# Optimization experiments

Measured on AMD Instinct MI355X. Metric: run time of the kernel, lower is better.

Reference implementation:

```python
import jax, jax.numpy as jnp
import numpy as np

K = 512
H = 8

def setup_inputs() -> dict:
    key = jax.random.key(0)
    k1, k2, k3, k4, k5 = jax.random.split(key, 5)
    b, s = 2, 2048
    x = jax.random.normal(k1, (b, s, K), dtype=jnp.float32)
    # torch Linear weights: shape [out_features, in_features]
    scale = 0.02
    Wq = jax.random.normal(k2, (H * K, K), dtype=jnp.float32) * scale
    Wk = jax.random.normal(k3, (H * K, K), dtype=jnp.float32) * scale
    Wv = jax.random.normal(k4, (H * K, K), dtype=jnp.float32) * scale
    Wu = jax.random.normal(k5, (K, H * K), dtype=jnp.float32) * scale
    return {"x": x, "Wq": Wq, "Wk": Wk, "Wv": Wv, "Wu": Wu}

def reference(x, Wq, Wk, Wv, Wu):
    b, s, _ = x.shape
    # project and split heads: [b, h, s, k]
    q = jnp.einsum('bsd,hed->bhse', x, Wq.reshape(H, K, K))
    kk = jnp.einsum('bsd,hed->bhse', x, Wk.reshape(H, K, K))
    v = jnp.einsum('bsd,hed->bhse', x, Wv.reshape(H, K, K))
    scale = K ** (-0.25)
    dot = jnp.einsum('bhse,bhte->bhst', q * scale, kk * scale)  # [b,h,s,s]
    causal = jnp.tril(jnp.ones((s, s), dtype=bool))
    dot = jnp.where(causal[None, None], dot, -jnp.inf)
    weights = jax.nn.softmax(dot, axis=-1)
    heads_out = jnp.einsum('bhst,bhte->bhse', weights, v)  # [b,h,s,k]
    heads_out = heads_out.transpose(0, 2, 1, 3).reshape(b, s, H * K)
    return heads_out @ Wu.T
```

## Files before the change

kernel.cpp:

```cpp
#include <hip/hip_runtime.h>
#include <hip/hip_bf16.h>
#include <cstdint>
#include <cstddef>


typedef __bf16 bf16;
typedef _Float16 f16;
typedef __bf16 bf16x8 __attribute__((ext_vector_type(8)));
typedef float  f32x4  __attribute__((ext_vector_type(4)));
typedef unsigned short u16x4 __attribute__((ext_vector_type(4)));

__device__ __forceinline__ void gl2lds16(const void* g, void* l) {
  __builtin_amdgcn_global_load_lds(
      (const __attribute__((address_space(1))) unsigned int*)g,
      (__attribute__((address_space(3))) unsigned int*)l, 16, 0, 0);
}

__device__ __forceinline__ unsigned short bfbits(float f) {
  return __builtin_bit_cast(unsigned short, (__bf16)f);
}
__device__ __forceinline__ float f16tof(unsigned short u) {
  return (float)__builtin_bit_cast(f16, u);
}

__global__ __launch_bounds__(256) void cvt_all(
    const float* __restrict__ x,  const float* __restrict__ wq,
    const float* __restrict__ wk, const float* __restrict__ wv,
    const float* __restrict__ wu,
    bf16* __restrict__ xb,  bf16* __restrict__ wqb, bf16* __restrict__ wkb,
    bf16* __restrict__ wvb, bf16* __restrict__ wub)
{
  const int Q4 = (1 << 21) / 4;
  int i = blockIdx.x * 256 + threadIdx.x;
  int a = i / Q4;
  int off = (i - a * Q4) * 4;
  const float* s; bf16* d;
  switch (a) {
    case 0: s = x;  d = xb;  break;
    case 1: s = wq; d = wqb; break;
    case 2: s = wk; d = wkb; break;
    case 3: s = wv; d = wvb; break;
    default: s = wu; d = wub; break;
  }
  float4 v = *(const float4*)(s + off);
  u16x4 o = { bfbits(v.x), bfbits(v.y), bfbits(v.z), bfbits(v.w) };
  *(u16x4*)(d + off) = o;
}

template<int BM, int BN, int MODE>
__global__ __launch_bounds__((BM / 64) * (BN / 64) * 64)
void gemm_bt(const bf16* __restrict__ A, const bf16* __restrict__ B,
             void* __restrict__ Cp, int M, int N, int K)
{
  constexpr int BK = 32;
  constexpr int WC = BN / 64;
  constexpr int NT = (BM / 64) * (BN / 64) * 64;
  __shared__ __align__(16) bf16 lds[2][(BM + BN) * BK];

  const int tid = threadIdx.x, w = tid >> 6, lane = tid & 63;
  const int g = lane >> 4, c16 = lane & 15;
  const int nbn = N / BN;
  const int bm = blockIdx.x / nbn, bn = blockIdx.x % nbn;
  const int m0 = bm * BM, n0 = bn * BN;
  const int wr = w / WC, wc = w % WC;

  f32x4 z = {0.f, 0.f, 0.f, 0.f};
  f32x4 acc[4][4];
  #pragma unroll
  for (int i = 0; i < 4; i++)
    #pragma unroll
    for (int j = 0; j < 4; j++) acc[i][j] = z;

  const int nk = K / BK;

  auto stage = [&](int buf, int kt) {
    bf16* la = &lds[buf][0];
    #pragma unroll
    for (int r = 0; r < (BM * BK / 8) / NT; r++) {
      int c = r * NT + tid;
      int row = c >> 2, p = c & 3, s = p ^ ((row >> 1) & 3);
      gl2lds16(A + (size_t)(m0 + row) * K + (size_t)kt * BK + s * 8,
               la + (r * NT + w * 64) * 8);
    }
    bf16* lb = &lds[buf][BM * BK];
    #pragma unroll
    for (int r = 0; r < (BN * BK / 8) / NT; r++) {
      int c = r * NT + tid;
      int row = c >> 2, p = c & 3, s = p ^ ((row >> 1) & 3);
      gl2lds16(B + (size_t)(n0 + row) * K + (size_t)kt * BK + s * 8,
               lb + (r * NT + w * 64) * 8);
    }
  };

  stage(0, 0);
  __syncthreads();
  int cur = 0;
  for (int kt = 0; kt < nk; ++kt) {
    if (kt + 1 < nk) stage(cur ^ 1, kt + 1);
    const bf16* lA = &lds[cur][0];
    const bf16* lB = &lds[cur][BM * BK];
    bf16x8 af[4], bfv[4];
    #pragma unroll
    for (int i = 0; i < 4; i++) {
      int ra = wr * 64 + i * 16 + c16;
      af[i] = *(const bf16x8*)&lA[ra * BK + ((g ^ ((ra >> 1) & 3)) * 8)];
      int rb = wc * 64 + i * 16 + c16;
      bfv[i] = *(const bf16x8*)&lB[rb * BK + ((g ^ ((rb >> 1) & 3)) * 8)];
    }
    #pragma unroll
    for (int i = 0; i < 4; i++)
      #pragma unroll
      for (int j = 0; j < 4; j++)
        acc[i][j] = __builtin_amdgcn_mfma_f32_16x16x32_bf16(af[i], bfv[j],
                                                            acc[i][j], 0, 0, 0);
    __syncthreads();
    cur ^= 1;
  }

  if constexpr (MODE == 0) {
    bf16* C = (bf16*)Cp;
    #pragma unroll
    for (int i = 0; i < 4; i++) {
      int mg = m0 + wr * 64 + i * 16 + g * 4;
      #pragma unroll
      for (int j = 0; j < 4; j++) {
        int ng = n0 + wc * 64 + j * 16 + c16;
        #pragma unroll
        for (int jj = 0; jj < 4; jj++)
          C[(size_t)(mg + jj) * N + ng] = (bf16)acc[i][j][jj];
      }
    }
  } else if constexpr (MODE == 1) {
    bf16* C = (bf16*)Cp;
    #pragma unroll
    for (int i = 0; i < 4; i++) {
      int mg = m0 + wr * 64 + i * 16 + g * 4;
      int bb = mg >> 11, srow = mg & 2047;
      #pragma unroll
      for (int j = 0; j < 4; j++) {
        int ng = n0 + wc * 64 + j * 16 + c16;
        u16x4 pk = { bfbits(acc[i][j][0]), bfbits(acc[i][j][1]),
                     bfbits(acc[i][j][2]), bfbits(acc[i][j][3]) };
        *(u16x4*)&C[(size_t)(bb * 4096 + ng) * 2048 + srow] = pk;
      }
    }
  } else {
    float* C = (float*)Cp;
    #pragma unroll
    for (int i = 0; i < 4; i++) {
      int mg = m0 + wr * 64 + i * 16 + g * 4;
      #pragma unroll
      for (int j = 0; j < 4; j++) {
        int ng = n0 + wc * 64 + j * 16 + c16;
        #pragma unroll
        for (int jj = 0; jj < 4; jj++)
          C[(size_t)(mg + jj) * N + ng] = acc[i][j][jj];
      }
    }
  }
}

__global__ __launch_bounds__(256)
void sgemm_causal(const bf16* __restrict__ Qb, const bf16* __restrict__ Kb,
                  f16* __restrict__ Sp)
{
  constexpr int BK = 32;
  __shared__ __align__(16) bf16 lds[2][256 * BK];
  const int tid = threadIdx.x, w = tid >> 6, lane = tid & 63;
  const int g = lane >> 4, c16 = lane & 15;

  const int bh = blockIdx.x / 136, t = blockIdx.x % 136;
  int tm = 0;
  while ((tm + 1) * (tm + 2) / 2 <= t) tm++;
  const int tn = t - tm * (tm + 1) / 2;
  const int b = bh >> 3, h = bh & 7;
  const bf16* Ab = Qb + (size_t)(b * 2048 + tm * 128) * 4096 + h * 512;
  const bf16* Bb = Kb + (size_t)(b * 2048 + tn * 128) * 4096 + h * 512;
  const int wr = w >> 1, wc = w & 1;

  f32x4 z = {0.f, 0.f, 0.f, 0.f};
  f32x4 acc[4][4];
  #pragma unroll
  for (int i = 0; i < 4; i++)
    #pragma unroll
    for (int j = 0; j < 4; j++) acc[i][j] = z;

  auto stage = [&](int buf, int kt) {
    bf16* la = &lds[buf][0];
    #pragma unroll
    for (int r = 0; r < 2; r++) {
      int c = r * 256 + tid;
      int row = c >> 2, p = c & 3, s = p ^ ((row >> 1) & 3);
      gl2lds16(Ab + (size_t)row * 4096 + kt * BK + s * 8,
               la + (r * 256 + w * 64) * 8);
    }
    bf16* lb = &lds[buf][128 * BK];
    #pragma unroll
    for (int r = 0; r < 2; r++) {
      int c = r * 256 + tid;
      int row = c >> 2, p = c & 3, s = p ^ ((row >> 1) & 3);
      gl2lds16(Bb + (size_t)row * 4096 + kt * BK + s * 8,
               lb + (r * 256 + w * 64) * 8);
    }
  };

  stage(0, 0);
  __syncthreads();
  int cur = 0;
  for (int kt = 0; kt < 16; ++kt) {
    if (kt + 1 < 16) stage(cur ^ 1, kt + 1);
    const bf16* lA = &lds[cur][0];
    const bf16* lB = &lds[cur][128 * BK];
    bf16x8 af[4], bfv[4];
    #pragma unroll
    for (int i = 0; i < 4; i++) {
      int ra = wr * 64 + i * 16 + c16;
      af[i] = *(const bf16x8*)&lA[ra * BK + ((g ^ ((ra >> 1) & 3)) * 8)];
      int rb = wc * 64 + i * 16 + c16;
      bfv[i] = *(const bf16x8*)&lB[rb * BK + ((g ^ ((rb >> 1) & 3)) * 8)];
    }
    #pragma unroll
    for (int i = 0; i < 4; i++)
      #pragma unroll
      for (int j = 0; j < 4; j++)
        acc[i][j] = __builtin_amdgcn_mfma_f32_16x16x32_bf16(af[i], bfv[j],
                                                            acc[i][j], 0, 0, 0);
    __syncthreads();
    cur ^= 1;
  }

  const float SC2 = 0.044194173824159216f * 1.4426950408889634f;
  f16* tb = Sp + ((size_t)bh * 136 + t) * 16384;
  #pragma unroll
  for (int i = 0; i < 4; i++) {
    int ml = wr * 64 + i * 16 + g * 4;
    #pragma unroll
    for (int j = 0; j < 4; j++) {
      int kl = wc * 64 + j * 16 + c16;
      #pragma unroll
      for (int jj = 0; jj < 4; jj++) {
        int ql = ml + jj;
        float v = acc[i][j][jj] * SC2;
        if (tn == tm && kl > ql) v = -30000.f;
        tb[ql * 128 + kl] = (f16)v;
      }
    }
  }
}

__global__ __launch_bounds__(256)
void softmax_rows(unsigned short* __restrict__ SP)
{
  const int w = threadIdx.x >> 6, lane = threadIdx.x & 63;
  const int W = blockIdx.x * 4 + w;
  #pragma unroll
  for (int pass = 0; pass < 2; ++pass) {
    int r = (pass == 0) ? W : (32767 - W);
    int bh = r >> 11, q = r & 2047;
    int tm = q >> 7, qr = q & 127;
    size_t rowb = ((size_t)bh * 136 + (size_t)tm * (tm + 1) / 2) * 16384
                  + (size_t)qr * 128 + lane * 2;
    unsigned int vals[16];
    float m = -3.0e38f;
    #pragma unroll
    for (int tn = 0; tn < 16; ++tn) {
      unsigned int u = 0xFC00FC00u;
      if (tn <= tm) u = *(const unsigned int*)(SP + rowb + (size_t)tn * 16384);
      vals[tn] = u;
      m = fmaxf(m, fmaxf(f16tof(u & 0xffff), f16tof(u >> 16)));
    }
    #pragma unroll
    for (int d = 1; d < 64; d <<= 1) m = fmaxf(m, __shfl_xor(m, d));
    float e0[16], e1[16], s = 0.f;
    #pragma unroll
    for (int tn = 0; tn < 16; ++tn) {
      e0[tn] = exp2f(f16tof(vals[tn] & 0xffff) - m);
      e1[tn] = exp2f(f16tof(vals[tn] >> 16) - m);
      s += e0[tn] + e1[tn];
    }
    #pragma unroll
    for (int d = 1; d < 64; d <<= 1) s += __shfl_xor(s, d);
    float inv = 1.f / s;
    #pragma unroll
    for (int tn = 0; tn < 16; ++tn) {
      if (tn <= tm) {
        unsigned int o = (unsigned)bfbits(e0[tn] * inv)
                       | ((unsigned)bfbits(e1[tn] * inv) << 16);
        *(unsigned int*)(SP + rowb + (size_t)tn * 16384) = o;
      }
    }
  }
}

__global__ __launch_bounds__(256)
void pv_gemm(const bf16* __restrict__ Pp, const bf16* __restrict__ Vt,
             bf16* __restrict__ HO)
{
  constexpr int BK = 32;
  __shared__ __align__(16) bf16 lds[2][256 * BK];
  const int tid = threadIdx.x, w = tid >> 6, lane = tid & 63;
  const int g = lane >> 4, c16 = lane & 15;

  const int idx = blockIdx.x;
  const int tm = 15 - (idx >> 6);
  const int r0 = idx & 63;
  const int bh = r0 >> 2, nd = r0 & 3;
  const int b = bh >> 3, h = bh & 7;
  const size_t pb = (size_t)bh * 136 + (size_t)tm * (tm + 1) / 2;
  const bf16* Bb = Vt + (size_t)(bh * 512 + nd * 128) * 2048;
  const int wr = w >> 1, wc = w & 1;
  const int nk = (tm + 1) * 4;

  f32x4 z = {0.f, 0.f, 0.f, 0.f};
  f32x4 acc[4][4];
  #pragma unroll
  for (int i = 0; i < 4; i++)
    #pragma unroll
    for (int j = 0; j < 4; j++) acc[i][j] = z;

  auto stage = [&](int buf, int kt) {
    const bf16* At = Pp + (pb + (kt >> 2)) * 16384 + (kt & 3) * 32;
    bf16* la = &lds[buf][0];
    #pragma unroll
    for (int r = 0; r < 2; r++) {
      int c = r * 256 + tid;
      int row = c >> 2, p = c & 3, s = p ^ ((row >> 1) & 3);
      gl2lds16(At + (size_t)row * 128 + s * 8,
               la + (r * 256 + w * 64) * 8);
    }
    bf16* lb = &lds[buf][128 * BK];
    #pragma unroll
    for (int r = 0; r < 2; r++) {
      int c = r * 256 + tid;
      int row = c >> 2, p = c & 3, s = p ^ ((row >> 1) & 3);
      gl2lds16(Bb + (size_t)row * 2048 + kt * BK + s * 8,
               lb + (r * 256 + w * 64) * 8);
    }
  };

  stage(0, 0);
  __syncthreads();
  int cur = 0;
  for (int kt = 0; kt < nk; ++kt) {
    if (kt + 1 < nk) stage(cur ^ 1, kt + 1);
    const bf16* lA = &lds[cur][0];
    const bf16* lB = &lds[cur][128 * BK];
    bf16x8 af[4], bfv[4];
    #pragma unroll
    for (int i = 0; i < 4; i++) {
      int ra = wr * 64 + i * 16 + c16;
      af[i] = *(const bf16x8*)&lA[ra * BK + ((g ^ ((ra >> 1) & 3)) * 8)];
      int rb = wc * 64 + i * 16 + c16;
      bfv[i] = *(const bf16x8*)&lB[rb * BK + ((g ^ ((rb >> 1) & 3)) * 8)];
    }
    #pragma unroll
    for (int i = 0; i < 4; i++)
      #pragma unroll
      for (int j = 0; j < 4; j++)
        acc[i][j] = __builtin_amdgcn_mfma_f32_16x16x32_bf16(af[i], bfv[j],
                                                            acc[i][j], 0, 0, 0);
    __syncthreads();
    cur ^= 1;
  }

  bf16* Cb = HO + (size_t)(b * 2048 + tm * 128) * 4096 + h * 512 + nd * 128;
  #pragma unroll
  for (int i = 0; i < 4; i++) {
    int ml = wr * 64 + i * 16 + g * 4;
    #pragma unroll
    for (int j = 0; j < 4; j++) {
      int nl = wc * 64 + j * 16 + c16;
      #pragma unroll
      for (int jj = 0; jj < 4; jj++)
        Cb[(size_t)(ml + jj) * 4096 + nl] = (bf16)acc[i][j][jj];
    }
  }
}

extern "C" void kernel_launch(void* const* d_in, const int* in_sizes, int n_in,
                              void* d_out, int out_size, void* d_ws,
                              size_t ws_size, hipStream_t stream)
{
  (void)in_sizes; (void)n_in; (void)out_size; (void)ws_size;
  const float* x  = (const float*)d_in[0];
  const float* wq = (const float*)d_in[1];
  const float* wk = (const float*)d_in[2];
  const float* wv = (const float*)d_in[3];
  const float* wu = (const float*)d_in[4];

  char* ws = (char*)d_ws;
  const size_t MB = 1024 * 1024;
  bf16* wub = (bf16*)(ws + 0 * MB);
  bf16* Qb  = (bf16*)(ws + 4 * MB);
  bf16* Kbf = (bf16*)(ws + 36 * MB);
  bf16* Vtb = (bf16*)(ws + 68 * MB);
  f16*  Sp  = (f16*)(ws + 100 * MB);
  bf16* xb  = (bf16*)(ws + 100 * MB);
  bf16* wqb = (bf16*)(ws + 104 * MB);
  bf16* wkb = (bf16*)(ws + 108 * MB);
  bf16* wvb = (bf16*)(ws + 112 * MB);
  bf16* HOb = Qb;

  hipLaunchKernelGGL(cvt_all, dim3(10240), dim3(256), 0, stream,
                     x, wq, wk, wv, wu, xb, wqb, wkb, wvb, wub);
  hipLaunchKernelGGL((gemm_bt<128, 128, 0>), dim3(1024), dim3(256), 0, stream,
                     xb, wqb, (void*)Qb, 4096, 4096, 512);
  hipLaunchKernelGGL((gemm_bt<128, 128, 0>), dim3(1024), dim3(256), 0, stream,
                     xb, wkb, (void*)Kbf, 4096, 4096, 512);
  hipLaunchKernelGGL((gemm_bt<128, 128, 1>), dim3(1024), dim3(256), 0, stream,
                     xb, wvb, (void*)Vtb, 4096, 4096, 512);
  hipLaunchKernelGGL(sgemm_causal, dim3(16 * 136), dim3(256), 0, stream,
                     Qb, Kbf, Sp);
  hipLaunchKernelGGL(softmax_rows, dim3(4096), dim3(256), 0, stream,
                     (unsigned short*)Sp);
  hipLaunchKernelGGL(pv_gemm, dim3(1024), dim3(256), 0, stream,
                     (const bf16*)Sp, Vtb, HOb);
  hipLaunchKernelGGL((gemm_bt<64, 128, 2>), dim3(256), dim3(128), 0, stream,
                     HOb, wub, d_out, 4096, 512, 4096);
}
```

Baseline: 412.3 us.

## Fuse softmax into score GEMM, enlarge tiles, swizzle blocks, defer normalization

The separate softmax pass is removed. The score GEMM now writes exp2 of the scaled scores directly, without subtracting the row max, and accumulates row sums with atomics. The PV GEMM divides by those sums in its epilogue. Tiles grow to 256x256 with 512 threads for the projection and score GEMMs, block indices are interleaved across XCDs, the workspace is remapped so V^T reuses the K buffer, and the final projection tile shape changes. Skipping the max subtraction risks overflow for larger logits, and the atomic sums make rounding order nondeterministic.

```diff
diff --git a/kernel.cpp b/kernel.cpp
--- a/kernel.cpp
+++ b/kernel.cpp
@@ -5,7 +5,6 @@
 
 
 typedef __bf16 bf16;
-typedef _Float16 f16;
 typedef __bf16 bf16x8 __attribute__((ext_vector_type(8)));
 typedef float  f32x4  __attribute__((ext_vector_type(4)));
 typedef unsigned short u16x4 __attribute__((ext_vector_type(4)));
@@ -18,9 +17,6 @@
 
 __device__ __forceinline__ unsigned short bfbits(float f) {
   return __builtin_bit_cast(unsigned short, (__bf16)f);
-}
-__device__ __forceinline__ float f16tof(unsigned short u) {
-  return (float)__builtin_bit_cast(f16, u);
 }
 
 __global__ __launch_bounds__(256) void cvt_all(
@@ -48,26 +44,31 @@
 }
 
 template<int BM, int BN, int MODE>
-__global__ __launch_bounds__((BM / 64) * (BN / 64) * 64)
+__global__ __launch_bounds__((BM >= 256 ? 2 : BM / 64) * (BN / 64) * 64)
 void gemm_bt(const bf16* __restrict__ A, const bf16* __restrict__ B,
              void* __restrict__ Cp, int M, int N, int K)
 {
   constexpr int BK = 32;
-  constexpr int WC = BN / 64;
-  constexpr int NT = (BM / 64) * (BN / 64) * 64;
+  constexpr int WM = (BM >= 256 ? 128 : 64);
+  constexpr int MI = WM / 16;
+  constexpr int WAVES_M = BM / WM;
+  constexpr int WAVES_N = BN / 64;
+  constexpr int NT = WAVES_M * WAVES_N * 64;
   __shared__ __align__(16) bf16 lds[2][(BM + BN) * BK];
 
   const int tid = threadIdx.x, w = tid >> 6, lane = tid & 63;
   const int g = lane >> 4, c16 = lane & 15;
+  const int q8 = gridDim.x >> 3;
+  const int wg = (blockIdx.x & 7) * q8 + (blockIdx.x >> 3);
   const int nbn = N / BN;
-  const int bm = blockIdx.x / nbn, bn = blockIdx.x % nbn;
+  const int bm = wg / nbn, bn = wg % nbn;
   const int m0 = bm * BM, n0 = bn * BN;
-  const int wr = w / WC, wc = w % WC;
+  const int wr = w / WAVES_N, wc = w % WAVES_N;
 
   f32x4 z = {0.f, 0.f, 0.f, 0.f};
-  f32x4 acc[4][4];
-  #pragma unroll
-  for (int i = 0; i < 4; i++)
+  f32x4 acc[MI][4];
+  #pragma unroll
+  for (int i = 0; i < MI; i++)
     #pragma unroll
     for (int j = 0; j < 4; j++) acc[i][j] = z;
 
@@ -99,16 +100,19 @@
     if (kt + 1 < nk) stage(cur ^ 1, kt + 1);
     const bf16* lA = &lds[cur][0];
     const bf16* lB = &lds[cur][BM * BK];
-    bf16x8 af[4], bfv[4];
-    #pragma unroll
-    for (int i = 0; i < 4; i++) {
-      int ra = wr * 64 + i * 16 + c16;
+    bf16x8 af[MI], bfv[4];
+    #pragma unroll
+    for (int i = 0; i < MI; i++) {
+      int ra = wr * WM + i * 16 + c16;
       af[i] = *(const bf16x8*)&lA[ra * BK + ((g ^ ((ra >> 1) & 3)) * 8)];
-      int rb = wc * 64 + i * 16 + c16;
-      bfv[i] = *(const bf16x8*)&lB[rb * BK + ((g ^ ((rb >> 1) & 3)) * 8)];
-    }
-    #pragma unroll
-    for (int i = 0; i < 4; i++)
+    }
+    #pragma unroll
+    for (int j = 0; j < 4; j++) {
+      int rb = wc * 64 + j * 16 + c16;
+      bfv[j] = *(const bf16x8*)&lB[rb * BK + ((g ^ ((rb >> 1) & 3)) * 8)];
+    }
+    #pragma unroll
+    for (int i = 0; i < MI; i++)
       #pragma unroll
       for (int j = 0; j < 4; j++)
         acc[i][j] = __builtin_amdgcn_mfma_f32_16x16x32_bf16(af[i], bfv[j],
@@ -120,8 +124,8 @@
   if constexpr (MODE == 0) {
     bf16* C = (bf16*)Cp;
     #pragma unroll
-    for (int i = 0; i < 4; i++) {
-      int mg = m0 + wr * 64 + i * 16 + g * 4;
+    for (int i = 0; i < MI; i++) {
+      int mg = m0 + wr * WM + i * 16 + g * 4;
       #pragma unroll
       for (int j = 0; j < 4; j++) {
         int ng = n0 + wc * 64 + j * 16 + c16;
@@ -133,8 +137,8 @@
   } else if constexpr (MODE == 1) {
     bf16* C = (bf16*)Cp;
     #pragma unroll
-    for (int i = 0; i < 4; i++) {
-      int mg = m0 + wr * 64 + i * 16 + g * 4;
+    for (int i = 0; i < MI; i++) {
+      int mg = m0 + wr * WM + i * 16 + g * 4;
       int bb = mg >> 11, srow = mg & 2047;
       #pragma unroll
       for (int j = 0; j < 4; j++) {
@@ -147,8 +151,8 @@
   } else {
     float* C = (float*)Cp;
     #pragma unroll
-    for (int i = 0; i < 4; i++) {
-      int mg = m0 + wr * 64 + i * 16 + g * 4;
+    for (int i = 0; i < MI; i++) {
+      int mg = m0 + wr * WM + i * 16 + g * 4;
       #pragma unroll
       for (int j = 0; j < 4; j++) {
         int ng = n0 + wc * 64 + j * 16 + c16;
@@ -160,28 +164,29 @@
   }
 }
 
-__global__ __launch_bounds__(256)
+__global__ __launch_bounds__(512)
 void sgemm_causal(const bf16* __restrict__ Qb, const bf16* __restrict__ Kb,
-                  f16* __restrict__ Sp)
+                  bf16* __restrict__ Sp, float* __restrict__ l)
 {
   constexpr int BK = 32;
-  __shared__ __align__(16) bf16 lds[2][256 * BK];
+  __shared__ __align__(16) bf16 lds[2][512 * BK];
   const int tid = threadIdx.x, w = tid >> 6, lane = tid & 63;
   const int g = lane >> 4, c16 = lane & 15;
 
-  const int bh = blockIdx.x / 136, t = blockIdx.x % 136;
-  int tm = 0;
-  while ((tm + 1) * (tm + 2) / 2 <= t) tm++;
-  const int tn = t - tm * (tm + 1) / 2;
+  const int wg = (blockIdx.x & 7) * 72 + (blockIdx.x >> 3);
+  const int bh = wg / 36, t = wg % 36;
+  int TM = 0;
+  while ((TM + 1) * (TM + 2) / 2 <= t) TM++;
+  const int TN = t - TM * (TM + 1) / 2;
   const int b = bh >> 3, h = bh & 7;
-  const bf16* Ab = Qb + (size_t)(b * 2048 + tm * 128) * 4096 + h * 512;
-  const bf16* Bb = Kb + (size_t)(b * 2048 + tn * 128) * 4096 + h * 512;
-  const int wr = w >> 1, wc = w & 1;
+  const bf16* Ab = Qb + (size_t)(b * 2048 + TM * 256) * 4096 + h * 512;
+  const bf16* Bb = Kb + (size_t)(b * 2048 + TN * 256) * 4096 + h * 512;
+  const int wr = w >> 2, wc = w & 3;
 
   f32x4 z = {0.f, 0.f, 0.f, 0.f};
-  f32x4 acc[4][4];
-  #pragma unroll
-  for (int i = 0; i < 4; i++)
+  f32x4 acc[8][4];
+  #pragma unroll
+  for (int i = 0; i < 8; i++)
     #pragma unroll
     for (int j = 0; j < 4; j++) acc[i][j] = z;
 
@@ -189,18 +194,18 @@
     bf16* la = &lds[buf][0];
     #pragma unroll
     for (int r = 0; r < 2; r++) {
-      int c = r * 256 + tid;
+      int c = r * 512 + tid;
       int row = c >> 2, p = c & 3, s = p ^ ((row >> 1) & 3);
       gl2lds16(Ab + (size_t)row * 4096 + kt * BK + s * 8,
-               la + (r * 256 + w * 64) * 8);
-    }
-    bf16* lb = &lds[buf][128 * BK];
+               la + (r * 512 + w * 64) * 8);
+    }
+    bf16* lb = &lds[buf][256 * BK];
     #pragma unroll
     for (int r = 0; r < 2; r++) {
-      int c = r * 256 + tid;
+      int c = r * 512 + tid;
       int row = c >> 2, p = c & 3, s = p ^ ((row >> 1) & 3);
       gl2lds16(Bb + (size_t)row * 4096 + kt * BK + s * 8,
-               lb + (r * 256 + w * 64) * 8);
+               lb + (r * 512 + w * 64) * 8);
     }
   };
 
@@ -210,17 +215,20 @@
   for (int kt = 0; kt < 16; ++kt) {
     if (kt + 1 < 16) stage(cur ^ 1, kt + 1);
     const bf16* lA = &lds[cur][0];
-    const bf16* lB = &lds[cur][128 * BK];
-    bf16x8 af[4], bfv[4];
-    #pragma unroll
-    for (int i = 0; i < 4; i++) {
-      int ra = wr * 64 + i * 16 + c16;
+    const bf16* lB = &lds[cur][256 * BK];
+    bf16x8 af[8], bfv[4];
+    #pragma unroll
+    for (int i = 0; i < 8; i++) {
+      int ra = wr * 128 + i * 16 + c16;
       af[i] = *(const bf16x8*)&lA[ra * BK + ((g ^ ((ra >> 1) & 3)) * 8)];
-      int rb = wc * 64 + i * 16 + c16;
-      bfv[i] = *(const bf16x8*)&lB[rb * BK + ((g ^ ((rb >> 1) & 3)) * 8)];
-    }
-    #pragma unroll
-    for (int i = 0; i < 4; i++)
+    }
+    #pragma unroll
+    for (int j = 0; j < 4; j++) {
+      int rb = wc * 64 + j * 16 + c16;
+      bfv[j] = *(const bf16x8*)&lB[rb * BK + ((g ^ ((rb >> 1) & 3)) * 8)];
+    }
+    #pragma unroll
+    for (int i = 0; i < 8; i++)
       #pragma unroll
       for (int j = 0; j < 4; j++)
         acc[i][j] = __builtin_amdgcn_mfma_f32_16x16x32_bf16(af[i], bfv[j],
@@ -230,85 +238,66 @@
   }
 
   const float SC2 = 0.044194173824159216f * 1.4426950408889634f;
-  f16* tb = Sp + ((size_t)bh * 136 + t) * 16384;
-  #pragma unroll
-  for (int i = 0; i < 4; i++) {
-    int ml = wr * 64 + i * 16 + g * 4;
+  bf16* spb = Sp + (size_t)bh * 136 * 16384;
+  float rsum[8][4];
+  #pragma unroll
+  for (int i = 0; i < 8; i++)
+    #pragma unroll
+    for (int jj = 0; jj < 4; jj++) rsum[i][jj] = 0.f;
+
+  #pragma unroll
+  for (int i = 0; i < 8; i++) {
     #pragma unroll
     for (int j = 0; j < 4; j++) {
       int kl = wc * 64 + j * 16 + c16;
+      int kglob = TN * 256 + kl;
+      int tn128 = kglob >> 7, kc = kglob & 127;
       #pragma unroll
       for (int jj = 0; jj < 4; jj++) {
-        int ql = ml + jj;
-        float v = acc[i][j][jj] * SC2;
-        if (tn == tm && kl > ql) v = -30000.f;
-        tb[ql * 128 + kl] = (f16)v;
+        int ml = wr * 128 + i * 16 + g * 4 + jj;
+        int qglob = TM * 256 + ml;
+        float p = (kglob <= qglob) ? exp2f(acc[i][j][jj] * SC2) : 0.f;
+        rsum[i][jj] += p;
+        int tm128 = qglob >> 7;
+        if (tn128 <= tm128)
+          spb[(size_t)(tm128 * (tm128 + 1) / 2 + tn128) * 16384
+              + (qglob & 127) * 128 + kc] = (bf16)p;
       }
     }
   }
-}
-
-__global__ __launch_bounds__(256)
-void softmax_rows(unsigned short* __restrict__ SP)
-{
-  const int w = threadIdx.x >> 6, lane = threadIdx.x & 63;
-  const int W = blockIdx.x * 4 + w;
-  #pragma unroll
-  for (int pass = 0; pass < 2; ++pass) {
-    int r = (pass == 0) ? W : (32767 - W);
-    int bh = r >> 11, q = r & 2047;
-    int tm = q >> 7, qr = q & 127;
-    size_t rowb = ((size_t)bh * 136 + (size_t)tm * (tm + 1) / 2) * 16384
-                  + (size_t)qr * 128 + lane * 2;
-    unsigned int vals[16];
-    float m = -3.0e38f;
-    #pragma unroll
-    for (int tn = 0; tn < 16; ++tn) {
-      unsigned int u = 0xFC00FC00u;
-      if (tn <= tm) u = *(const unsigned int*)(SP + rowb + (size_t)tn * 16384);
-      vals[tn] = u;
-      m = fmaxf(m, fmaxf(f16tof(u & 0xffff), f16tof(u >> 16)));
-    }
-    #pragma unroll
-    for (int d = 1; d < 64; d <<= 1) m = fmaxf(m, __shfl_xor(m, d));
-    float e0[16], e1[16], s = 0.f;
-    #pragma unroll
-    for (int tn = 0; tn < 16; ++tn) {
-      e0[tn] = exp2f(f16tof(vals[tn] & 0xffff) - m);
-      e1[tn] = exp2f(f16tof(vals[tn] >> 16) - m);
-      s += e0[tn] + e1[tn];
-    }
-    #pragma unroll
-    for (int d = 1; d < 64; d <<= 1) s += __shfl_xor(s, d);
-    float inv = 1.f / s;
-    #pragma unroll
-    for (int tn = 0; tn < 16; ++tn) {
-      if (tn <= tm) {
-        unsigned int o = (unsigned)bfbits(e0[tn] * inv)
-                       | ((unsigned)bfbits(e1[tn] * inv) << 16);
-        *(unsigned int*)(SP + rowb + (size_t)tn * 16384) = o;
+  #pragma unroll
+  for (int i = 0; i < 8; i++)
+    #pragma unroll
+    for (int jj = 0; jj < 4; jj++) {
+      float v = rsum[i][jj];
+      v += __shfl_xor(v, 1);
+      v += __shfl_xor(v, 2);
+      v += __shfl_xor(v, 4);
+      v += __shfl_xor(v, 8);
+      if (c16 == 0) {
+        int qglob = TM * 256 + wr * 128 + i * 16 + g * 4 + jj;
+        atomicAdd(&l[bh * 2048 + qglob], v);
       }
     }
-  }
-}
-
-__global__ __launch_bounds__(256)
+}
+
+__global__ __launch_bounds__(512)
 void pv_gemm(const bf16* __restrict__ Pp, const bf16* __restrict__ Vt,
-             bf16* __restrict__ HO)
+             const float* __restrict__ l, bf16* __restrict__ HO)
 {
   constexpr int BK = 32;
-  __shared__ __align__(16) bf16 lds[2][256 * BK];
+  __shared__ __align__(16) bf16 lds[2][384 * BK];
+  __shared__ float sInv[128];
   const int tid = threadIdx.x, w = tid >> 6, lane = tid & 63;
   const int g = lane >> 4, c16 = lane & 15;
 
-  const int idx = blockIdx.x;
-  const int tm = 15 - (idx >> 6);
-  const int r0 = idx & 63;
-  const int bh = r0 >> 2, nd = r0 & 3;
+  const int wg = (blockIdx.x & 7) * 64 + (blockIdx.x >> 3);
+  const int bh = wg >> 5, r5 = wg & 31;
+  const int tm = 15 - (r5 >> 1), nd = r5 & 1;
   const int b = bh >> 3, h = bh & 7;
   const size_t pb = (size_t)bh * 136 + (size_t)tm * (tm + 1) / 2;
-  const bf16* Bb = Vt + (size_t)(bh * 512 + nd * 128) * 2048;
-  const int wr = w >> 1, wc = w & 1;
+  const bf16* Bb = Vt + (size_t)(bh * 512 + nd * 256) * 2048;
+  const int wr = w >> 2, wc = w & 3;
   const int nk = (tm + 1) * 4;
 
   f32x4 z = {0.f, 0.f, 0.f, 0.f};
@@ -321,24 +310,22 @@
   auto stage = [&](int buf, int kt) {
     const bf16* At = Pp + (pb + (kt >> 2)) * 16384 + (kt & 3) * 32;
     bf16* la = &lds[buf][0];
+    {
+      int row = tid >> 2, p = tid & 3, s = p ^ ((row >> 1) & 3);
+      gl2lds16(At + (size_t)row * 128 + s * 8, la + (w * 64) * 8);
+    }
+    bf16* lb = &lds[buf][128 * BK];
     #pragma unroll
     for (int r = 0; r < 2; r++) {
-      int c = r * 256 + tid;
-      int row = c >> 2, p = c & 3, s = p ^ ((row >> 1) & 3);
-      gl2lds16(At + (size_t)row * 128 + s * 8,
-               la + (r * 256 + w * 64) * 8);
-    }
-    bf16* lb = &lds[buf][128 * BK];
-    #pragma unroll
-    for (int r = 0; r < 2; r++) {
-      int c = r * 256 + tid;
+      int c = r * 512 + tid;
       int row = c >> 2, p = c & 3, s = p ^ ((row >> 1) & 3);
       gl2lds16(Bb + (size_t)row * 2048 + kt * BK + s * 8,
-               lb + (r * 256 + w * 64) * 8);
+               lb + (r * 512 + w * 64) * 8);
     }
   };
 
   stage(0, 0);
+  if (tid < 128) sInv[tid] = 1.0f / l[bh * 2048 + tm * 128 + tid];
   __syncthreads();
   int cur = 0;
   for (int kt = 0; kt < nk; ++kt) {
@@ -350,8 +337,11 @@
     for (int i = 0; i < 4; i++) {
       int ra = wr * 64 + i * 16 + c16;
       af[i] = *(const bf16x8*)&lA[ra * BK + ((g ^ ((ra >> 1) & 3)) * 8)];
-      int rb = wc * 64 + i * 16 + c16;
-      bfv[i] = *(const bf16x8*)&lB[rb * BK + ((g ^ ((rb >> 1) & 3)) * 8)];
+    }
+    #pragma unroll
+    for (int j = 0; j < 4; j++) {
+      int rb = wc * 64 + j * 16 + c16;
+      bfv[j] = *(const bf16x8*)&lB[rb * BK + ((g ^ ((rb >> 1) & 3)) * 8)];
     }
     #pragma unroll
     for (int i = 0; i < 4; i++)
@@ -363,7 +353,7 @@
     cur ^= 1;
   }
 
-  bf16* Cb = HO + (size_t)(b * 2048 + tm * 128) * 4096 + h * 512 + nd * 128;
+  bf16* Cb = HO + (size_t)(b * 2048 + tm * 128) * 4096 + h * 512 + nd * 256;
   #pragma unroll
   for (int i = 0; i < 4; i++) {
     int ml = wr * 64 + i * 16 + g * 4;
@@ -372,7 +362,8 @@
       int nl = wc * 64 + j * 16 + c16;
       #pragma unroll
       for (int jj = 0; jj < 4; jj++)
-        Cb[(size_t)(ml + jj) * 4096 + nl] = (bf16)acc[i][j][jj];
+        Cb[(size_t)(ml + jj) * 4096 + nl] =
+            (bf16)(acc[i][j][jj] * sInv[ml + jj]);
     }
   }
 }
@@ -390,31 +381,31 @@
 
   char* ws = (char*)d_ws;
   const size_t MB = 1024 * 1024;
-  bf16* wub = (bf16*)(ws + 0 * MB);
-  bf16* Qb  = (bf16*)(ws + 4 * MB);
-  bf16* Kbf = (bf16*)(ws + 36 * MB);
-  bf16* Vtb = (bf16*)(ws + 68 * MB);
-  f16*  Sp  = (f16*)(ws + 100 * MB);
-  bf16* xb  = (bf16*)(ws + 100 * MB);
-  bf16* wqb = (bf16*)(ws + 104 * MB);
-  bf16* wkb = (bf16*)(ws + 108 * MB);
-  bf16* wvb = (bf16*)(ws + 112 * MB);
-  bf16* HOb = Qb;
-
+  bf16*  wub = (bf16*)(ws + 0 * MB);
+  float* lR  = (float*)(ws + 4 * MB);
+  bf16*  Qb  = (bf16*)(ws + 5 * MB);
+  bf16*  Kbf = (bf16*)(ws + 37 * MB);
+  bf16*  Sp  = (bf16*)(ws + 69 * MB);
+  bf16*  wqb = (bf16*)(ws + 69 * MB);
+  bf16*  wkb = (bf16*)(ws + 73 * MB);
+  bf16*  xb  = (bf16*)(ws + 137 * MB);
+  bf16*  wvb = (bf16*)(ws + 141 * MB);
+  bf16*  Vtb = Kbf;
+  bf16*  HOb = Qb;
+
+  hipMemsetAsync(lR, 0, 16 * 2048 * sizeof(float), stream);
   hipLaunchKernelGGL(cvt_all, dim3(10240), dim3(256), 0, stream,
                      x, wq, wk, wv, wu, xb, wqb, wkb, wvb, wub);
-  hipLaunchKernelGGL((gemm_bt<128, 128, 0>), dim3(1024), dim3(256), 0, stream,
+  hipLaunchKernelGGL((gemm_bt<256, 256, 0>), dim3(256), dim3(512), 0, stream,
                      xb, wqb, (void*)Qb, 4096, 4096, 512);
-  hipLaunchKernelGGL((gemm_bt<128, 128, 0>), dim3(1024), dim3(256), 0, stream,
+  hipLaunchKernelGGL((gemm_bt<256, 256, 0>), dim3(256), dim3(512), 0, stream,
                      xb, wkb, (void*)Kbf, 4096, 4096, 512);
-  hipLaunchKernelGGL((gemm_bt<128, 128, 1>), dim3(1024), dim3(256), 0, stream,
+  hipLaunchKernelGGL(sgemm_causal, dim3(576), dim3(512), 0, stream,
+                     Qb, Kbf, Sp, lR);
+  hipLaunchKernelGGL((gemm_bt<256, 256, 1>), dim3(256), dim3(512), 0, stream,
                      xb, wvb, (void*)Vtb, 4096, 4096, 512);
-  hipLaunchKernelGGL(sgemm_causal, dim3(16 * 136), dim3(256), 0, stream,
-                     Qb, Kbf, Sp);
-  hipLaunchKernelGGL(softmax_rows, dim3(4096), dim3(256), 0, stream,
-                     (unsigned short*)Sp);
-  hipLaunchKernelGGL(pv_gemm, dim3(1024), dim3(256), 0, stream,
-                     (const bf16*)Sp, Vtb, HOb);
-  hipLaunchKernelGGL((gemm_bt<64, 128, 2>), dim3(256), dim3(128), 0, stream,
+  hipLaunchKernelGGL(pv_gemm, dim3(512), dim3(512), 0, stream,
+                     Sp, Vtb, lR, HOb);
+  hipLaunchKernelGGL((gemm_bt<128, 64, 2>), dim3(256), dim3(128), 0, stream,
                      HOb, wub, d_out, 4096, 512, 4096);
 }
```

New measurement: 371.7 us. -9.8%, faster.
